# Optimization experiments

Hardware: AMD Instinct MI355X
Metric: run time of the kernel (lower is better)

Reference implementation:

```python
import jax, jax.numpy as jnp
import numpy as np

B = 8192
D1 = 1024
D2 = 1024
H = 4096  # subnet hidden width
SCALE_LIMIT = 1.0


def _mlp(x, W1, b1, W2, b2):
    # Linear -> ReLU -> Linear
    return jnp.maximum(x @ W1 + b1, 0.0) @ W2 + b2


def setup_inputs() -> dict:
    key = jax.random.key(0)
    ks = jax.random.split(key, 17)
    inp = {"x": jax.random.normal(ks[0], (B, D1 + D2), dtype=jnp.float32)}
    # four subnets: s1,t1 map d2->d1 ; s2,t2 map d1->d2
    specs = {"s1": (D2, D1), "t1": (D2, D1), "s2": (D1, D2), "t2": (D1, D2)}
    i = 1
    for name, (din, dout) in specs.items():
        inp[f"{name}_W1"] = 0.02 * jax.random.normal(ks[i], (din, H), dtype=jnp.float32); i += 1
        inp[f"{name}_b1"] = jnp.zeros((H,), dtype=jnp.float32)
        inp[f"{name}_W2"] = 0.02 * jax.random.normal(ks[i], (H, dout), dtype=jnp.float32); i += 1
        inp[f"{name}_b2"] = jnp.zeros((dout,), dtype=jnp.float32)
    return inp


def reference(x,
              s1_W1, s1_b1, s1_W2, s1_b2,
              t1_W1, t1_b1, t1_W2, t1_b2,
              s2_W1, s2_b1, s2_W2, s2_b2,
              t2_W1, t2_b1, t2_W2, t2_b2):
    x1, x2 = x[:, :D1], x[:, D1:]
    # first half-step: update x1 conditioned on x2
    s2v = jnp.tanh(_mlp(x2, s1_W1, s1_b1, s1_W2, s1_b2)) * SCALE_LIMIT  # [B, D1]
    t2v = _mlp(x2, t1_W1, t1_b1, t1_W2, t1_b2)                          # [B, D1]
    y1 = x1 * jnp.exp(s2v) + t2v
    # second half-step: update x2 conditioned on y1
    s1v = jnp.tanh(_mlp(y1, s2_W1, s2_b1, s2_W2, s2_b2)) * SCALE_LIMIT  # [B, D2]
    t1v = _mlp(y1, t2_W1, t2_b1, t2_W2, t2_b2)                          # [B, D2]
    y2 = x2 * jnp.exp(s1v) + t1v
    y = jnp.concatenate([y1, y2], axis=1)  # [B, D1+D2]
    # exact triangular-coupling log-det (what the autograd loop computes per-sample)
    log_det = jnp.sum(s2v, axis=1) + jnp.sum(s1v, axis=1)  # [B]
    return y, log_det
```

## Files before the change

### kernel.cpp

```cpp
#include <hip/hip_runtime.h>
#include <cstdint>
#include <cstddef>

#define BDIM 8192
#define D1 1024
#define HDIM 4096

typedef __attribute__((ext_vector_type(8))) short short8;
typedef __attribute__((ext_vector_type(4))) float f32x4;
typedef __attribute__((ext_vector_type(4))) unsigned short u16x4;

__device__ inline void async_load16(const void* g, void* l) {
  __builtin_amdgcn_global_load_lds(
      (const __attribute__((address_space(1))) void*)g,
      (__attribute__((address_space(3))) void*)l,
      16 , 0 , 0 );
}

__device__ inline unsigned short f2bf(float f) {
  union { float f; uint32_t u; } v; v.f = f;
  uint32_t u = v.u;
  uint32_t r = u + 0x7FFFu + ((u >> 16) & 1u);
  return (unsigned short)(r >> 16);
}
__device__ inline float bf2f(unsigned short u) {
  union { uint32_t u; float f; } v; v.u = (uint32_t)u << 16; return v.f;
}

__global__ __launch_bounds__(512, 2)
void gemm8(const unsigned short* __restrict__ A0,
           const unsigned short* __restrict__ A1, int lda,
           const unsigned short* __restrict__ B0,
           const unsigned short* __restrict__ B1,
           const float* __restrict__ bias0, const float* __restrict__ bias1,
           unsigned short* __restrict__ C0, unsigned short* __restrict__ C1,
           int ldc, int K, int relu) {
  __shared__ __align__(16) unsigned short smem[65536];

  const int z = blockIdx.z;
  const unsigned short* A  = z ? A1 : A0;
  const unsigned short* Bw = z ? B1 : B0;
  const float* biasP       = z ? bias1 : bias0;
  unsigned short* C        = z ? C1 : C0;

  const int nX  = gridDim.x;
  const int nwg = gridDim.x * gridDim.y;
  const int bid = blockIdx.y * gridDim.x + blockIdx.x;
  const int q = nwg >> 3, r = nwg & 7;
  const int xcd = bid & 7, rest = bid >> 3;
  const int wg = (xcd < r ? xcd * (q + 1) : r * (q + 1) + (xcd - r) * q) + rest;
  const int tm = wg / nX, tn = wg % nX;
  const int m0 = tm * 256, n0 = tn * 256;

  const int tid  = threadIdx.x;
  const int wave = tid >> 6, lane = tid & 63;
  const int quad = lane >> 4, l15 = lane & 15;
  const int wm = wave >> 2, wn = wave & 3;

  const int sr    = tid >> 2;
  const int sslot = (tid & 3) ^ ((tid >> 3) & 3);
  const unsigned short* gA = A  + (long)(m0 + sr) * lda + sslot * 8;
  const unsigned short* gB = Bw + (long)(n0 + sr) * K   + sslot * 8;

  const int swz = ((quad ^ ((l15 >> 1) & 3)) << 3);
  const unsigned short* aB = smem + wm * 4096  + l15 * 32 + swz;
  const unsigned short* bB = smem + 32768 + wn * 2048 + l15 * 32 + swz;

  f32x4 acc[8][4] = {};
  const int NT = K >> 6;

#define STAGE_A(NB, SL, KT) { \
  unsigned short* lw = smem + (NB)*16384 + (SL)*8192 + wave*512; \
  const unsigned short* g = gA + (long)(KT)*64 + (SL)*32; \
  async_load16(g, lw); \
  async_load16(g + 128*(long)lda, lw + 4096); }

#define STAGE_B(NB, SL, KT) { \
  unsigned short* lw = smem + 32768 + (NB)*16384 + (SL)*8192 + wave*512; \
  const unsigned short* g = gB + (long)(KT)*64 + (SL)*32; \
  async_load16(g, lw); \
  async_load16(g + 128*(long)K, lw + 4096); }

#define READ_A(dst, BUF, SL, MH) { \
  const unsigned short* p = aB + (BUF)*16384 + (SL)*8192 + (MH)*2048; \
  dst[0] = *(const short8*)(p);        dst[1] = *(const short8*)(p + 512); \
  dst[2] = *(const short8*)(p + 1024); dst[3] = *(const short8*)(p + 1536); }

#define READ_B(dst, BUF, SL) { \
  const unsigned short* p = bB + (BUF)*16384 + (SL)*8192; \
  dst[0] = *(const short8*)(p);        dst[1] = *(const short8*)(p + 512); \
  dst[2] = *(const short8*)(p + 1024); dst[3] = *(const short8*)(p + 1536); }

#define MFMA16(MH, AV, BV) \
  _Pragma("unroll") \
  for (int mt = 0; mt < 4; ++mt) { \
    _Pragma("unroll") \
    for (int nt = 0; nt < 4; ++nt) { \
      acc[(MH)*4 + mt][nt] = __builtin_amdgcn_mfma_f32_16x16x32_bf16( \
          AV[mt], BV[nt], acc[(MH)*4 + mt][nt], 0, 0, 0); \
    } }

#define BARRIER() asm volatile("s_barrier" ::: "memory")
#define VMCNT4()  asm volatile("s_waitcnt vmcnt(4)" ::: "memory")

#define TILE_BODY(BUF, NB, TNX) { \
  short8 a0[4], a1[4], b0v[4], b1v[4]; \
   \
  READ_A(a0, BUF, 0, 0); READ_B(b0v, BUF, 0); \
  STAGE_A(NB, 0, TNX); \
  BARRIER(); \
  __builtin_amdgcn_s_setprio(1); MFMA16(0, a0, b0v); __builtin_amdgcn_s_setprio(0); \
   \
  READ_A(a1, BUF, 0, 1); \
  STAGE_B(NB, 0, TNX); \
  VMCNT4(); \
  BARRIER(); \
  __builtin_amdgcn_s_setprio(1); MFMA16(1, a1, b0v); __builtin_amdgcn_s_setprio(0); \
   \
  READ_A(a0, BUF, 1, 0); READ_B(b1v, BUF, 1); \
  STAGE_A(NB, 1, TNX); \
  BARRIER(); \
  __builtin_amdgcn_s_setprio(1); MFMA16(0, a0, b1v); __builtin_amdgcn_s_setprio(0); \
   \
  READ_A(a1, BUF, 1, 1); \
  STAGE_B(NB, 1, TNX); \
  VMCNT4(); \
  BARRIER(); \
  __builtin_amdgcn_s_setprio(1); MFMA16(1, a1, b1v); __builtin_amdgcn_s_setprio(0); \
}

  STAGE_A(0, 0, 0); STAGE_B(0, 0, 0); STAGE_A(0, 1, 0); STAGE_B(0, 1, 0);
  VMCNT4();
  BARRIER();

#pragma unroll 1
  for (int t = 0; t < NT; t += 2) {
    const int tnx1 = t + 1;
    const int tnx2 = (t + 2 < NT) ? t + 2 : NT - 1;
    TILE_BODY(0, 1, tnx1);
    TILE_BODY(1, 0, tnx2);
  }

  asm volatile("s_waitcnt vmcnt(0)" ::: "memory");
  BARRIER();

  unsigned short* sc = smem + wave * 8192;
#pragma unroll
  for (int nt = 0; nt < 4; ++nt) {
    const int col = n0 + wn * 64 + nt * 16 + l15;
    const float bv = biasP[col];
#pragma unroll
    for (int mt = 0; mt < 8; ++mt) {
#pragma unroll
      for (int rr = 0; rr < 4; ++rr) {
        const int lrow = mt * 16 + quad * 4 + rr;
        float v = acc[mt][nt][rr] + bv;
        if (relu) v = v > 0.f ? v : 0.f;
        sc[lrow * 64 + ((nt * 16 + l15) ^ (((lrow >> 2) & 3) << 4))] = f2bf(v);
      }
    }
  }
  const long rowbase = m0 + wm * 128;
  const int colbase  = n0 + wn * 64;
#pragma unroll
  for (int i = 0; i < 16; ++i) {
    const int L   = i * 1024 + lane * 16;
    const int row = L >> 7;
    const int sp  = (L & 127) >> 4;
    const int cg  = sp ^ ((((row) >> 2) & 3) << 1);
    short8 v = *(const short8*)&sc[row * 64 + sp * 8];
    *(short8*)&C[(rowbase + row) * (long)ldc + colbase + cg * 8] = v;
  }

#undef STAGE_A
#undef STAGE_B
#undef READ_A
#undef READ_B
#undef MFMA16
#undef BARRIER
#undef VMCNT4
#undef TILE_BODY
}

__global__ __launch_bounds__(256)
void couple(const unsigned short* sb, const unsigned short* __restrict__ tb,
            const float* __restrict__ x, float* __restrict__ y,
            unsigned short* y1b, float* __restrict__ ld,
            long growoff, int xoff, int addld) {
  __shared__ float wsum[4];
  const int row = blockIdx.x;
  const long grow = growoff + row;
  const int c = threadIdx.x * 4;

  u16x4 sv4 = *(const u16x4*)&sb[(long)row * 1024 + c];
  u16x4 tv4 = *(const u16x4*)&tb[(long)row * 1024 + c];
  f32x4 xv  = *(const f32x4*)&x[grow * 2048 + xoff + c];
  f32x4 yv;
  unsigned short yb[4];
  float rs = 0.f;
#pragma unroll
  for (int j = 0; j < 4; ++j) {
    float s  = bf2f(sv4[j]);
    float t  = bf2f(tv4[j]);
    float sv = tanhf(s);
    rs += sv;
    float yy = xv[j] * __expf(sv) + t;
    yv[j] = yy;
    yb[j] = f2bf(yy);
  }
  *(f32x4*)&y[grow * 2048 + xoff + c] = yv;
  if (y1b) {
    u16x4 o; o[0] = yb[0]; o[1] = yb[1]; o[2] = yb[2]; o[3] = yb[3];
    *(u16x4*)&y1b[(long)row * 1024 + c] = o;
  }
#pragma unroll
  for (int o = 32; o > 0; o >>= 1) rs += __shfl_down(rs, o);
  const int wv = threadIdx.x >> 6, ln = threadIdx.x & 63;
  if (ln == 0) wsum[wv] = rs;
  __syncthreads();
  if (threadIdx.x == 0) {
    float tot = wsum[0] + wsum[1] + wsum[2] + wsum[3];
    if (addld) ld[grow] += tot; else ld[grow] = tot;
  }
}

__global__ __launch_bounds__(256)
void transpose_cast(const float* __restrict__ in, unsigned short* __restrict__ out,
                    int R, int C) {
  __shared__ float tile[32][33];
  const int bx = blockIdx.x * 32;
  const int by = blockIdx.y * 32;
  const int tx = threadIdx.x & 31;
  const int ty = threadIdx.x >> 5;
  for (int j = ty; j < 32; j += 8)
    tile[j][tx] = in[(long)(by + j) * C + bx + tx];
  __syncthreads();
  for (int j = ty; j < 32; j += 8)
    out[(long)(bx + j) * R + by + tx] = f2bf(tile[tx][j]);
}

__global__ __launch_bounds__(256)
void cast_x2(const float* __restrict__ x, unsigned short* __restrict__ x2b) {
  long i = (long)blockIdx.x * 256 + threadIdx.x;
  long row = i >> 10, col = i & 1023;
  x2b[i] = f2bf(x[row * (2 * D1) + D1 + col]);
}

extern "C" void kernel_launch(void* const* d_in, const int* in_sizes, int n_in,
                              void* d_out, int out_size, void* d_ws, size_t ws_size,
                              hipStream_t stream) {
  const float* x     = (const float*)d_in[0];
  const float* s1_W1 = (const float*)d_in[1];
  const float* s1_b1 = (const float*)d_in[2];
  const float* s1_W2 = (const float*)d_in[3];
  const float* s1_b2 = (const float*)d_in[4];
  const float* t1_W1 = (const float*)d_in[5];
  const float* t1_b1 = (const float*)d_in[6];
  const float* t1_W2 = (const float*)d_in[7];
  const float* t1_b2 = (const float*)d_in[8];
  const float* s2_W1 = (const float*)d_in[9];
  const float* s2_b1 = (const float*)d_in[10];
  const float* s2_W2 = (const float*)d_in[11];
  const float* s2_b2 = (const float*)d_in[12];
  const float* t2_W1 = (const float*)d_in[13];
  const float* t2_b1 = (const float*)d_in[14];
  const float* t2_W2 = (const float*)d_in[15];
  const float* t2_b2 = (const float*)d_in[16];

  const size_t MB = 1024UL * 1024UL;
  float* y_out  = (float*)d_out;
  float* ld_out = (float*)d_out + (long)BDIM * (2 * D1);
  char* ws = (char*)d_ws;

  if (ws_size >= 192 * MB) {
    unsigned short* w1a = (unsigned short*)(ws + 0 * MB);
    unsigned short* w1b = (unsigned short*)(ws + 8 * MB);
    unsigned short* w2a = (unsigned short*)(ws + 16 * MB);
    unsigned short* w2b = (unsigned short*)(ws + 24 * MB);
    unsigned short* x2b = (unsigned short*)(ws + 32 * MB);
    unsigned short* tb  = (unsigned short*)(ws + 48 * MB);
    unsigned short* h   = (unsigned short*)(ws + 64 * MB);

    cast_x2<<<(BDIM * D1) / 256, 256, 0, stream>>>(x, x2b);
    transpose_cast<<<dim3(HDIM / 32, D1 / 32), 256, 0, stream>>>(s1_W1, w1a, D1, HDIM);
    transpose_cast<<<dim3(HDIM / 32, D1 / 32), 256, 0, stream>>>(t1_W1, w1b, D1, HDIM);
    transpose_cast<<<dim3(D1 / 32, HDIM / 32), 256, 0, stream>>>(s1_W2, w2a, HDIM, D1);
    transpose_cast<<<dim3(D1 / 32, HDIM / 32), 256, 0, stream>>>(t1_W2, w2b, HDIM, D1);

    gemm8<<<dim3(16, 32, 2), 512, 0, stream>>>(x2b, x2b, D1, w1a, w1b,
        s1_b1, t1_b1, h, h + 4096, 2 * HDIM, D1, 1);
    transpose_cast<<<dim3(HDIM / 32, D1 / 32), 256, 0, stream>>>(s2_W1, w1a, D1, HDIM);
    transpose_cast<<<dim3(HDIM / 32, D1 / 32), 256, 0, stream>>>(t2_W1, w1b, D1, HDIM);
    gemm8<<<dim3(4, 32, 2), 512, 0, stream>>>(h, h + 4096, 2 * HDIM, w2a, w2b,
        s1_b2, t1_b2, x2b , tb, D1, HDIM, 0);
    transpose_cast<<<dim3(D1 / 32, HDIM / 32), 256, 0, stream>>>(s2_W2, w2a, HDIM, D1);
    transpose_cast<<<dim3(D1 / 32, HDIM / 32), 256, 0, stream>>>(t2_W2, w2b, HDIM, D1);
    couple<<<BDIM, 256, 0, stream>>>(x2b, tb, x, y_out, x2b ,
                                     ld_out, 0, 0, 0);
    gemm8<<<dim3(16, 32, 2), 512, 0, stream>>>(x2b, x2b, D1, w1a, w1b,
        s2_b1, t2_b1, h, h + 4096, 2 * HDIM, D1, 1);
    gemm8<<<dim3(4, 32, 2), 512, 0, stream>>>(h, h + 4096, 2 * HDIM, w2a, w2b,
        s2_b2, t2_b2, x2b , tb, D1, HDIM, 0);
    couple<<<BDIM, 256, 0, stream>>>(x2b, tb, x, y_out, nullptr, ld_out, 0, D1, 1);
  } else {
    int NC = 2;
    while (NC < 16) {
      size_t need = 80 * MB + (16 * MB) / NC + (128 * MB) / NC;
      if (need <= ws_size) break;
      NC <<= 1;
    }
    const int Mrows = BDIM / NC;
    unsigned short* w1s1 = (unsigned short*)(ws + 0 * MB);
    unsigned short* w1t1 = (unsigned short*)(ws + 8 * MB);
    unsigned short* w1s2 = (unsigned short*)(ws + 16 * MB);
    unsigned short* w1t2 = (unsigned short*)(ws + 24 * MB);
    unsigned short* w2s1 = (unsigned short*)(ws + 32 * MB);
    unsigned short* w2t1 = (unsigned short*)(ws + 40 * MB);
    unsigned short* w2s2 = (unsigned short*)(ws + 48 * MB);
    unsigned short* w2t2 = (unsigned short*)(ws + 56 * MB);
    unsigned short* x2b  = (unsigned short*)(ws + 64 * MB);
    unsigned short* tb   = (unsigned short*)(ws + 80 * MB);
    unsigned short* h    = (unsigned short*)(ws + 80 * MB + (16 * MB) / NC);

    cast_x2<<<(BDIM * D1) / 256, 256, 0, stream>>>(x, x2b);
    transpose_cast<<<dim3(HDIM / 32, D1 / 32), 256, 0, stream>>>(s1_W1, w1s1, D1, HDIM);
    transpose_cast<<<dim3(HDIM / 32, D1 / 32), 256, 0, stream>>>(t1_W1, w1t1, D1, HDIM);
    transpose_cast<<<dim3(HDIM / 32, D1 / 32), 256, 0, stream>>>(s2_W1, w1s2, D1, HDIM);
    transpose_cast<<<dim3(HDIM / 32, D1 / 32), 256, 0, stream>>>(t2_W1, w1t2, D1, HDIM);
    transpose_cast<<<dim3(D1 / 32, HDIM / 32), 256, 0, stream>>>(s1_W2, w2s1, HDIM, D1);
    transpose_cast<<<dim3(D1 / 32, HDIM / 32), 256, 0, stream>>>(t1_W2, w2t1, HDIM, D1);
    transpose_cast<<<dim3(D1 / 32, HDIM / 32), 256, 0, stream>>>(s2_W2, w2s2, HDIM, D1);
    transpose_cast<<<dim3(D1 / 32, HDIM / 32), 256, 0, stream>>>(t2_W2, w2t2, HDIM, D1);

    for (int c = 0; c < NC; ++c) {
      const long moff = (long)c * Mrows;
      unsigned short* xA = x2b + moff * D1;
      gemm8<<<dim3(16, Mrows / 256, 2), 512, 0, stream>>>(xA, xA, D1, w1s1, w1t1,
          s1_b1, t1_b1, h, h + 4096, 2 * HDIM, D1, 1);
      gemm8<<<dim3(4, Mrows / 256, 2), 512, 0, stream>>>(h, h + 4096, 2 * HDIM,
          w2s1, w2t1, s1_b2, t1_b2, xA, tb, D1, HDIM, 0);
      couple<<<Mrows, 256, 0, stream>>>(xA, tb, x, y_out, xA, ld_out, moff, 0, 0);
      gemm8<<<dim3(16, Mrows / 256, 2), 512, 0, stream>>>(xA, xA, D1, w1s2, w1t2,
          s2_b1, t2_b1, h, h + 4096, 2 * HDIM, D1, 1);
      gemm8<<<dim3(4, Mrows / 256, 2), 512, 0, stream>>>(h, h + 4096, 2 * HDIM,
          w2s2, w2t2, s2_b2, t2_b2, xA, tb, D1, HDIM, 0);
      couple<<<Mrows, 256, 0, stream>>>(xA, tb, x, y_out, nullptr, ld_out, moff, D1, 1);
    }
  }
}
```

Measured before the change: 763.7 us.

## Drop GEMM barriers, batch weight transposes, add single-pass large-workspace path

Removes two of the four s_barrier calls per tile body in the GEMM main loop, so MFMA work can start without waiting on the whole block after A staging. Merges the eight per-weight transpose/cast launches into two launches that use a z-dimension index to pick the matrix. Adds a new top-priority path for workspaces of at least 224 MB that holds all eight transposed weights at once and processes the whole batch without chunking. Removing the barriers risks LDS read/write races between waves if staging overwrites buffers that are still being read.

```diff
diff --git a/kernel.cpp b/kernel.cpp
--- a/kernel.cpp
+++ b/kernel.cpp
@@ -108,7 +108,6 @@
    \
   READ_A(a0, BUF, 0, 0); READ_B(b0v, BUF, 0); \
   STAGE_A(NB, 0, TNX); \
-  BARRIER(); \
   __builtin_amdgcn_s_setprio(1); MFMA16(0, a0, b0v); __builtin_amdgcn_s_setprio(0); \
    \
   READ_A(a1, BUF, 0, 1); \
@@ -119,7 +118,6 @@
    \
   READ_A(a0, BUF, 1, 0); READ_B(b1v, BUF, 1); \
   STAGE_A(NB, 1, TNX); \
-  BARRIER(); \
   __builtin_amdgcn_s_setprio(1); MFMA16(0, a0, b1v); __builtin_amdgcn_s_setprio(0); \
    \
   READ_A(a1, BUF, 1, 1); \
@@ -228,6 +226,27 @@
 void transpose_cast(const float* __restrict__ in, unsigned short* __restrict__ out,
                     int R, int C) {
   __shared__ float tile[32][33];
+  const int bx = blockIdx.x * 32;
+  const int by = blockIdx.y * 32;
+  const int tx = threadIdx.x & 31;
+  const int ty = threadIdx.x >> 5;
+  for (int j = ty; j < 32; j += 8)
+    tile[j][tx] = in[(long)(by + j) * C + bx + tx];
+  __syncthreads();
+  for (int j = ty; j < 32; j += 8)
+    out[(long)(bx + j) * R + by + tx] = f2bf(tile[tx][j]);
+}
+
+__global__ __launch_bounds__(256)
+void transpose_cast4(const float* __restrict__ s0, const float* __restrict__ s1,
+                     const float* __restrict__ s2, const float* __restrict__ s3,
+                     unsigned short* __restrict__ d0, unsigned short* __restrict__ d1,
+                     unsigned short* __restrict__ d2, unsigned short* __restrict__ d3,
+                     int R, int C) {
+  __shared__ float tile[32][33];
+  const int bz = blockIdx.z;
+  const float* in = bz == 0 ? s0 : bz == 1 ? s1 : bz == 2 ? s2 : s3;
+  unsigned short* out = bz == 0 ? d0 : bz == 1 ? d1 : bz == 2 ? d2 : d3;
   const int bx = blockIdx.x * 32;
   const int by = blockIdx.y * 32;
   const int tx = threadIdx.x & 31;
@@ -272,7 +291,37 @@
   float* ld_out = (float*)d_out + (long)BDIM * (2 * D1);
   char* ws = (char*)d_ws;
 
-  if (ws_size >= 192 * MB) {
+  if (ws_size >= 224 * MB) {
+    unsigned short* w1s1 = (unsigned short*)(ws + 0 * MB);
+    unsigned short* w1t1 = (unsigned short*)(ws + 8 * MB);
+    unsigned short* w1s2 = (unsigned short*)(ws + 16 * MB);
+    unsigned short* w1t2 = (unsigned short*)(ws + 24 * MB);
+    unsigned short* w2s1 = (unsigned short*)(ws + 32 * MB);
+    unsigned short* w2t1 = (unsigned short*)(ws + 40 * MB);
+    unsigned short* w2s2 = (unsigned short*)(ws + 48 * MB);
+    unsigned short* w2t2 = (unsigned short*)(ws + 56 * MB);
+    unsigned short* x2b  = (unsigned short*)(ws + 64 * MB);
+    unsigned short* tb   = (unsigned short*)(ws + 80 * MB);
+    unsigned short* h    = (unsigned short*)(ws + 96 * MB);
+
+    cast_x2<<<(BDIM * D1) / 256, 256, 0, stream>>>(x, x2b);
+    transpose_cast4<<<dim3(HDIM / 32, D1 / 32, 4), 256, 0, stream>>>(
+        s1_W1, t1_W1, s2_W1, t2_W1, w1s1, w1t1, w1s2, w1t2, D1, HDIM);
+    transpose_cast4<<<dim3(D1 / 32, HDIM / 32, 4), 256, 0, stream>>>(
+        s1_W2, t1_W2, s2_W2, t2_W2, w2s1, w2t1, w2s2, w2t2, HDIM, D1);
+
+    gemm8<<<dim3(16, 32, 2), 512, 0, stream>>>(x2b, x2b, D1, w1s1, w1t1,
+        s1_b1, t1_b1, h, h + 4096, 2 * HDIM, D1, 1);
+    gemm8<<<dim3(4, 32, 2), 512, 0, stream>>>(h, h + 4096, 2 * HDIM, w2s1, w2t1,
+        s1_b2, t1_b2, x2b , tb, D1, HDIM, 0);
+    couple<<<BDIM, 256, 0, stream>>>(x2b, tb, x, y_out, x2b ,
+                                     ld_out, 0, 0, 0);
+    gemm8<<<dim3(16, 32, 2), 512, 0, stream>>>(x2b, x2b, D1, w1s2, w1t2,
+        s2_b1, t2_b1, h, h + 4096, 2 * HDIM, D1, 1);
+    gemm8<<<dim3(4, 32, 2), 512, 0, stream>>>(h, h + 4096, 2 * HDIM, w2s2, w2t2,
+        s2_b2, t2_b2, x2b , tb, D1, HDIM, 0);
+    couple<<<BDIM, 256, 0, stream>>>(x2b, tb, x, y_out, nullptr, ld_out, 0, D1, 1);
+  } else if (ws_size >= 192 * MB) {
     unsigned short* w1a = (unsigned short*)(ws + 0 * MB);
     unsigned short* w1b = (unsigned short*)(ws + 8 * MB);
     unsigned short* w2a = (unsigned short*)(ws + 16 * MB);
@@ -323,14 +372,10 @@
     unsigned short* h    = (unsigned short*)(ws + 80 * MB + (16 * MB) / NC);
 
     cast_x2<<<(BDIM * D1) / 256, 256, 0, stream>>>(x, x2b);
-    transpose_cast<<<dim3(HDIM / 32, D1 / 32), 256, 0, stream>>>(s1_W1, w1s1, D1, HDIM);
-    transpose_cast<<<dim3(HDIM / 32, D1 / 32), 256, 0, stream>>>(t1_W1, w1t1, D1, HDIM);
-    transpose_cast<<<dim3(HDIM / 32, D1 / 32), 256, 0, stream>>>(s2_W1, w1s2, D1, HDIM);
-    transpose_cast<<<dim3(HDIM / 32, D1 / 32), 256, 0, stream>>>(t2_W1, w1t2, D1, HDIM);
-    transpose_cast<<<dim3(D1 / 32, HDIM / 32), 256, 0, stream>>>(s1_W2, w2s1, HDIM, D1);
-    transpose_cast<<<dim3(D1 / 32, HDIM / 32), 256, 0, stream>>>(t1_W2, w2t1, HDIM, D1);
-    transpose_cast<<<dim3(D1 / 32, HDIM / 32), 256, 0, stream>>>(s2_W2, w2s2, HDIM, D1);
-    transpose_cast<<<dim3(D1 / 32, HDIM / 32), 256, 0, stream>>>(t2_W2, w2t2, HDIM, D1);
+    transpose_cast4<<<dim3(HDIM / 32, D1 / 32, 4), 256, 0, stream>>>(
+        s1_W1, t1_W1, s2_W1, t2_W1, w1s1, w1t1, w1s2, w1t2, D1, HDIM);
+    transpose_cast4<<<dim3(D1 / 32, HDIM / 32, 4), 256, 0, stream>>>(
+        s1_W2, t1_W2, s2_W2, t2_W2, w2s1, w2t1, w2s2, w2t2, HDIM, D1);
 
     for (int c = 0; c < NC; ++c) {
       const long moff = (long)c * Mrows;
```

Result: slower. 793.5 us (+3.9%).
